# Kernel optimization log

Hardware: AMD Instinct MI355X
Metric: run time of the kernel (lower is better)

## Reference

```python
import jax, jax.numpy as jnp
import numpy as np

B, R, M, L, H = 256, 2048, 65536, 64, 4  # batch, reservoir, memory_size, key_len, read_heads


def setup_inputs() -> dict:
    key = jax.random.key(0)
    ks = jax.random.split(key, 4)
    s = 1.0 / np.sqrt(R).astype(np.float32)  # ~xavier scale for Linear weights
    return {
        "reservoir_state": jax.random.normal(ks[0], (B, R), dtype=jnp.float32),
        "memory": jax.random.normal(ks[1], (1, M, L), dtype=jnp.float32),
        "Wk": jax.random.normal(ks[2], (H * L, R), dtype=jnp.float32) * s,
        "bk": jnp.zeros((H * L,), dtype=jnp.float32),
        "Wb": jax.random.normal(ks[3], (H, R), dtype=jnp.float32) * s,
        "bb": jnp.zeros((H,), dtype=jnp.float32),
    }


def reference(reservoir_state, memory, Wk, bk, Wb, bb):
    b = reservoir_state.shape[0]
    h = Wb.shape[0]
    # key projection -> [B, H, L]
    keys = (reservoir_state @ Wk.T + bk).reshape(b, h, -1)
    # per-head key strength, relu-gated -> [B, H]
    betas = jax.nn.relu(reservoir_state @ Wb.T + bb)
    # content addressing: dot(keys, memory rows) -> [B, H, M]
    dots = jnp.einsum('bhl,ml->bhm', keys, memory[0])
    # normalize by key norm (as in original: sqrt(sum(keys^2)))
    dots = dots / jnp.sqrt(jnp.sum(keys ** 2, axis=-1, keepdims=True))
    # beta-scaled softmax over memory slots
    return jax.nn.softmax(betas[:, :, None] * dots, axis=-1)
```

## Files before the change

kernel.cpp:

```cpp
#include <hip/hip_runtime.h>
#include <hip/hip_bf16.h>

#define BB   256
#define RR   2048
#define MM   65536
#define LL   64
#define HH   4
#define NROW 1024
#define KEYS 256

typedef float f32x4 __attribute__((ext_vector_type(4)));
typedef short short8 __attribute__((ext_vector_type(8)));

#define MFMA(A,B,C) __builtin_amdgcn_mfma_f32_16x16x32_bf16((A),(B),(C),0,0,0)
#define LOG2E 1.4426950408889634f
#define EXP2F(x) __builtin_amdgcn_exp2f(x)

__device__ __forceinline__ void lds_barrier() {
    asm volatile("s_waitcnt lgkmcnt(0)" ::: "memory");
    __builtin_amdgcn_sched_barrier(0);
    __builtin_amdgcn_s_barrier();
    __builtin_amdgcn_sched_barrier(0);
}

__device__ __forceinline__ unsigned short bf16_rn(float x) {
    union { float f; unsigned int u; } v; v.f = x;
    unsigned int r = v.u + 0x7FFFu + ((v.u >> 16) & 1u);
    return (unsigned short)(r >> 16);
}
__device__ __forceinline__ float bf16_to_f(unsigned short h) {
    union { float f; unsigned int u; } v; v.u = ((unsigned int)h) << 16; return v.f;
}
__device__ __forceinline__ void split8_store(const float* x, unsigned short* hi, unsigned short* lo) {
    unsigned int ph[4], pl[4];
#pragma unroll
    for (int j = 0; j < 4; ++j) {
        unsigned short h0 = bf16_rn(x[2*j]),   l0 = bf16_rn(x[2*j]   - bf16_to_f(h0));
        unsigned short h1 = bf16_rn(x[2*j+1]), l1 = bf16_rn(x[2*j+1] - bf16_to_f(h1));
        ph[j] = (unsigned int)h0 | ((unsigned int)h1 << 16);
        pl[j] = (unsigned int)l0 | ((unsigned int)l1 << 16);
    }
    ((uint4*)hi)[0] = make_uint4(ph[0], ph[1], ph[2], ph[3]);
    ((uint4*)lo)[0] = make_uint4(pl[0], pl[1], pl[2], pl[3]);
}
__device__ __forceinline__ void split8_reg(const float* x, short8& hi, short8& lo) {
    union { unsigned int u[4]; short8 s; } H, L;
#pragma unroll
    for (int j = 0; j < 4; ++j) {
        unsigned short h0 = bf16_rn(x[2*j]),   l0 = bf16_rn(x[2*j]   - bf16_to_f(h0));
        unsigned short h1 = bf16_rn(x[2*j+1]), l1 = bf16_rn(x[2*j+1] - bf16_to_f(h1));
        H.u[j] = (unsigned int)h0 | ((unsigned int)h1 << 16);
        L.u[j] = (unsigned int)l0 | ((unsigned int)l1 << 16);
    }
    hi = H.s; lo = L.s;
}

__global__ __launch_bounds__(256) void setup_k(const float* __restrict__ mem,
                                               const float* __restrict__ Wk,
                                               const float* __restrict__ S,
                                               unsigned short* __restrict__ bhi,
                                               unsigned short* __restrict__ blo,
                                               float* __restrict__ normpart,
                                               float* __restrict__ kpart) {
    __shared__ float sh[18496];
    int bx = blockIdx.x, tid = threadIdx.x;
    if (bx < 512) {
        float* t     = sh;
        float* rowsq = sh + 128 * 68;
        int blk = bx;
        const f32x4* src = (const f32x4*)(mem + (size_t)blk * 128 * LL);
#pragma unroll
        for (int i = 0; i < 8; ++i) {
            int idx = i * 256 + tid;
            int row = idx >> 4, c4 = idx & 15;
            *(f32x4*)&t[row * 68 + c4 * 4] = src[idx];
        }
        __syncthreads();
        if (tid < 128) {
            const float* rp = t + tid * 68;
            float s = 0.f;
#pragma unroll
            for (int k = 0; k < 64; ++k) s = fmaf(rp[k], rp[k], s);
            rowsq[tid] = s;
        }
        __syncthreads();
        if (tid < 64) {
            float m = fmaxf(rowsq[tid], rowsq[tid + 64]);
#pragma unroll
            for (int off = 1; off < 64; off <<= 1) m = fmaxf(m, __shfl_xor(m, off, 64));
            if (tid == 0) normpart[blk] = m;
        }
#pragma unroll
        for (int i = 0; i < 4; ++i) {
            int slot = i * 256 + tid;
            int lane = slot & 63, frag_l = slot >> 6;
            int t_l = frag_l >> 1, c = frag_l & 1;
            int row = t_l * 16 + (lane & 15);
            int k0 = c * 32 + (lane >> 4) * 8;
            const float* p = t + row * 68 + k0;
            float x[8];
#pragma unroll
            for (int j = 0; j < 8; ++j) x[j] = p[j];
            size_t gslot = ((size_t)blk * 16 + frag_l) * 64 + lane;
            split8_store(x, bhi + gslot * 8, blo + gslot * 8);
        }
    } else {
        float* sl = sh;
        float* wk = sh + 2048;
        int bx2 = bx - 512;
        int bg = bx2 >> 3, kc = bx2 & 7;
        int b0 = bg * 8;
#pragma unroll
        for (int bi = 0; bi < 8; ++bi)
            sl[bi * 256 + tid] = S[(size_t)(b0 + bi) * RR + kc * 256 + tid];
        float acc[8] = {0,0,0,0,0,0,0,0};
        for (int sub = 0; sub < 4; ++sub) {
            const f32x4* wsrc = (const f32x4*)(Wk + (size_t)tid * RR + kc * 256 + sub * 64);
#pragma unroll
            for (int i = 0; i < 16; ++i) {
                f32x4 v = wsrc[i];
#pragma unroll
                for (int q = 0; q < 4; ++q)
                    wk[(i * 4 + q) * 257 + tid] = v[q];
            }
            __syncthreads();
#pragma unroll 4
            for (int kkl = 0; kkl < 64; ++kkl) {
                float wv = wk[kkl * 257 + tid];
                int kk = sub * 64 + kkl;
#pragma unroll
                for (int bi = 0; bi < 8; ++bi)
                    acc[bi] = fmaf(sl[bi * 256 + kk], wv, acc[bi]);
            }
            __syncthreads();
        }
        float* op = kpart + (size_t)kc * BB * KEYS + (size_t)b0 * KEYS + tid;
#pragma unroll
        for (int bi = 0; bi < 8; ++bi)
            op[bi * KEYS] = acc[bi];
    }
}

__global__ __launch_bounds__(256) void k1_finalize(const float* __restrict__ S,
                                                   const float* __restrict__ kpart,
                                                   const float* __restrict__ bk,
                                                   const float* __restrict__ Wb,
                                                   const float* __restrict__ bb,
                                                   const float* __restrict__ normpart,
                                                   float* __restrict__ q_rm,
                                                   float* __restrict__ brow) {
    int bh = blockIdx.x, b = bh >> 2, h = bh & 3;
    int tid = threadIdx.x, lane = tid & 63, w = tid >> 6;
    float p = 0.f;
#pragma unroll
    for (int i = 0; i < 8; ++i) {
        int k = i * 256 + tid;
        p += S[(size_t)b * RR + k] * Wb[(size_t)h * RR + k];
    }
    float nm = fmaxf(normpart[tid], normpart[256 + tid]);
#pragma unroll
    for (int off = 1; off < 64; off <<= 1) {
        p  += __shfl_xor(p, off, 64);
        nm  = fmaxf(nm, __shfl_xor(nm, off, 64));
    }
    __shared__ float red[4], redm[4];
    if (lane == 0) { red[w] = p; redm[w] = nm; }
    __syncthreads();
    if (tid < 64) {
        float beta = red[0] + red[1] + red[2] + red[3] + bb[h];
        beta = fmaxf(beta, 0.f);
        float maxn = sqrtf(fmaxf(fmaxf(redm[0], redm[1]), fmaxf(redm[2], redm[3])));
        float kv = bk[h * LL + lane];
#pragma unroll
        for (int c = 0; c < 8; ++c)
            kv += kpart[(size_t)c * BB * KEYS + (size_t)b * KEYS + h * LL + lane];
        float sq = kv * kv;
#pragma unroll
        for (int off = 1; off < 64; off <<= 1) sq += __shfl_xor(sq, off, 64);
        float scale = beta * LOG2E / sqrtf(sq);
        q_rm[(size_t)bh * LL + lane] = kv * scale;
        if (lane == 0) brow[bh] = beta * maxn * LOG2E;
    }
}

__device__ __forceinline__ void decode_wg(int bx, int& mblk, int& rg) {
    int wg = ((bx & 7) << 7) | (bx >> 3);
    mblk = wg >> 4; rg = wg & 15;
}

__global__ __launch_bounds__(256) void k2_mfma(const unsigned short* __restrict__ bhi,
                                               const unsigned short* __restrict__ blo,
                                               const float* __restrict__ q_rm,
                                               const float* __restrict__ brow,
                                               float* __restrict__ psum) {
    int mblk, rg; decode_wg(blockIdx.x, mblk, rg);
    int tid = threadIdx.x, w = tid >> 6, lane = tid & 63;
    int g = lane >> 4;
    short8 Ah[4][2], Al[4][2];
#pragma unroll
    for (int rt = 0; rt < 4; ++rt)
#pragma unroll
        for (int c = 0; c < 2; ++c) {
            const float* qp = q_rm + (size_t)(rg * 64 + rt * 16 + (lane & 15)) * LL
                              + c * 32 + (lane >> 4) * 8;
            f32x4 x0 = *(const f32x4*)qp, x1 = *(const f32x4*)(qp + 4);
            float x[8] = {x0[0], x0[1], x0[2], x0[3], x1[0], x1[1], x1[2], x1[3]};
            split8_reg(x, Ah[rt][c], Al[rt][c]);
        }
    float br[4][4];
#pragma unroll
    for (int rt = 0; rt < 4; ++rt)
#pragma unroll
        for (int r = 0; r < 4; ++r)
            br[rt][r] = brow[rg * 64 + rt * 16 + g * 4 + r];
    float s[4][4] = {{0.f}};
    int t0 = mblk * 64 + w * 16;
    short8 Bh0, Bh1, Bl0, Bl1;
    {
        size_t o = (size_t)t0 * 1024 + (size_t)lane * 8;
        Bh0 = *(const short8*)(bhi + o); Bh1 = *(const short8*)(bhi + o + 512);
        Bl0 = *(const short8*)(blo + o); Bl1 = *(const short8*)(blo + o + 512);
    }
#pragma unroll 4
    for (int ti = 0; ti < 16; ++ti) {
        int tn = t0 + ((ti < 15) ? ti + 1 : 15);
        size_t on = (size_t)tn * 1024 + (size_t)lane * 8;
        short8 nh0 = *(const short8*)(bhi + on);
        short8 nh1 = *(const short8*)(bhi + on + 512);
        short8 nl0 = *(const short8*)(blo + on);
        short8 nl1 = *(const short8*)(blo + on + 512);
#pragma unroll
        for (int rt = 0; rt < 4; ++rt) {
            f32x4 C = {0.f, 0.f, 0.f, 0.f};
            C = MFMA(Ah[rt][0], Bh0, C);
            C = MFMA(Ah[rt][1], Bh1, C);
            C = MFMA(Al[rt][0], Bh0, C);
            C = MFMA(Al[rt][1], Bh1, C);
            C = MFMA(Ah[rt][0], Bl0, C);
            C = MFMA(Ah[rt][1], Bl1, C);
#pragma unroll
            for (int r = 0; r < 4; ++r)
                s[rt][r] += EXP2F(C[r] - br[rt][r]);
        }
        Bh0 = nh0; Bh1 = nh1; Bl0 = nl0; Bl1 = nl1;
    }
#pragma unroll
    for (int rt = 0; rt < 4; ++rt)
#pragma unroll
        for (int r = 0; r < 4; ++r) {
            float v = s[rt][r];
            v += __shfl_xor(v, 1, 64);
            v += __shfl_xor(v, 2, 64);
            v += __shfl_xor(v, 4, 64);
            v += __shfl_xor(v, 8, 64);
            s[rt][r] = v;
        }
    if ((lane & 15) == 0) {
        int col = mblk * 4 + w;
#pragma unroll
        for (int rt = 0; rt < 4; ++rt)
#pragma unroll
            for (int r = 0; r < 4; ++r) {
                int row = rg * 64 + rt * 16 + g * 4 + r;
                psum[(size_t)row * 256 + col] = s[rt][r];
            }
    }
}

__global__ __launch_bounds__(256) void k4_mfma(const unsigned short* __restrict__ bhi,
                                               const unsigned short* __restrict__ blo,
                                               const float* __restrict__ q_rm,
                                               const float* __restrict__ brow,
                                               const float* __restrict__ psum,
                                               float* __restrict__ out) {
    __shared__ float ot[16 * 516];
    __shared__ float gsh[16];
    int bx = blockIdx.x;
    int wg = ((bx & 7) << 7) | (bx >> 3);
    int mblk = wg >> 6, rg = wg & 63;
    int tid = threadIdx.x, w = tid >> 6, lane = tid & 63;
    int g = lane >> 4;
    {
        int row16 = tid >> 4, seg = tid & 15;
        const float* pp = psum + (size_t)(rg * 16 + row16) * 256 + seg * 16;
        float part = 0.f;
#pragma unroll
        for (int j = 0; j < 16; ++j) part += pp[j];
#pragma unroll
        for (int off = 1; off < 16; off <<= 1) part += __shfl_xor(part, off, 64);
        if (seg == 0) gsh[row16] = 1.0f / part;
    }
    short8 Ah[2], Al[2];
#pragma unroll
    for (int c = 0; c < 2; ++c) {
        const float* qp = q_rm + (size_t)(rg * 16 + (lane & 15)) * LL
                          + c * 32 + (lane >> 4) * 8;
        f32x4 x0 = *(const f32x4*)qp, x1 = *(const f32x4*)(qp + 4);
        float x[8] = {x0[0], x0[1], x0[2], x0[3], x1[0], x1[1], x1[2], x1[3]};
        split8_reg(x, Ah[c], Al[c]);
    }
    __syncthreads();
    float br[4], gv[4];
#pragma unroll
    for (int r = 0; r < 4; ++r) {
        int row = rg * 16 + g * 4 + r;
        br[r] = brow[row];
        gv[r] = gsh[g * 4 + r];
    }
    int tbase = mblk * 256 + w * 8;
    short8 Bh0, Bh1, Bl0, Bl1;
    {
        size_t o = (size_t)tbase * 1024 + (size_t)lane * 8;
        Bh0 = *(const short8*)(bhi + o); Bh1 = *(const short8*)(bhi + o + 512);
        Bl0 = *(const short8*)(blo + o); Bl1 = *(const short8*)(blo + o + 512);
    }
    for (int c = 0; c < 8; ++c) {
#pragma unroll
        for (int k = 0; k < 8; ++k) {
            int j = c * 8 + k;
            int jn = (j < 63) ? j + 1 : 63;
            int tn = tbase + (jn >> 3) * 32 + (jn & 7);
            size_t on = (size_t)tn * 1024 + (size_t)lane * 8;
            short8 nh0 = *(const short8*)(bhi + on);
            short8 nh1 = *(const short8*)(bhi + on + 512);
            short8 nl0 = *(const short8*)(blo + on);
            short8 nl1 = *(const short8*)(blo + on + 512);
            f32x4 C = {0.f, 0.f, 0.f, 0.f};
            C = MFMA(Ah[0], Bh0, C);
            C = MFMA(Ah[1], Bh1, C);
            C = MFMA(Al[0], Bh0, C);
            C = MFMA(Al[1], Bh1, C);
            C = MFMA(Ah[0], Bl0, C);
            C = MFMA(Ah[1], Bl1, C);
            int cbase = w * 128 + k * 16 + (lane & 15);
#pragma unroll
            for (int r = 0; r < 4; ++r)
                ot[(g * 4 + r) * 516 + cbase] = EXP2F(C[r] - br[r]) * gv[r];
            Bh0 = nh0; Bh1 = nh1; Bl0 = nl0; Bl1 = nl1;
        }
        lds_barrier();
        size_t gbase = (size_t)mblk * 4096 + (size_t)c * 512;
#pragma unroll
        for (int i = 0; i < 8; ++i) {
            int flat = i * 256 + tid;
            int rl = flat >> 7, slot = flat & 127;
            f32x4 v = *(const f32x4*)&ot[rl * 516 + slot * 4];
            float* dst = out + (size_t)(rg * 16 + rl) * MM + gbase + (size_t)slot * 4;
            __builtin_nontemporal_store(v, (f32x4*)dst);
        }
        lds_barrier();
    }
}

extern "C" void kernel_launch(void* const* d_in, const int* in_sizes, int n_in,
                              void* d_out, int out_size, void* d_ws, size_t ws_size,
                              hipStream_t stream) {
    const float* S   = (const float*)d_in[0];
    const float* mem = (const float*)d_in[1];
    const float* Wk  = (const float*)d_in[2];
    const float* bk  = (const float*)d_in[3];
    const float* Wb  = (const float*)d_in[4];
    const float* bb  = (const float*)d_in[5];
    float* out = (float*)d_out;

    float* kpart    = (float*)d_ws;
    float* q_rm     = kpart + (size_t)8 * BB * KEYS;
    float* psum     = q_rm  + (size_t)NROW * LL;
    float* brow     = psum  + (size_t)NROW * 256;
    float* normpart = brow  + NROW;
    unsigned short* bhi = (unsigned short*)(normpart + 512);
    unsigned short* blo = bhi + (size_t)8192 * 512;

    setup_k    <<<768,  256, 0, stream>>>(mem, Wk, S, bhi, blo, normpart, kpart);
    k1_finalize<<<NROW, 256, 0, stream>>>(S, kpart, bk, Wb, bb, normpart, q_rm, brow);
    k2_mfma    <<<1024, 256, 0, stream>>>(bhi, blo, q_rm, brow, psum);
    k4_mfma    <<<1024, 256, 0, stream>>>(bhi, blo, q_rm, brow, psum, out);
}
```

Before: 359.2 us.

## Retile k4 to 64 query rows per block for memory-tile reuse

The output kernel now processes 64 query rows per workgroup instead of 16, covering half as many memory slots per block, and launches 512 blocks instead of 1024. Each loaded bf16 hi/lo memory fragment feeds four row-tiles of MFMAs, cutting repeated global reads of the memory matrix by about four times. The cost is more registers for the A fragments and the per-row constants, a larger LDS staging buffer, and fewer blocks. That may reduce occupancy on a store-bound kernel.

```diff
diff --git a/kernel.cpp b/kernel.cpp
--- a/kernel.cpp
+++ b/kernel.cpp
@@ -273,41 +273,46 @@
                                                const float* __restrict__ brow,
                                                const float* __restrict__ psum,
                                                float* __restrict__ out) {
-    __shared__ float ot[16 * 516];
-    __shared__ float gsh[16];
+    __shared__ float ot[64 * 260];
+    __shared__ float gsh[64];
     int bx = blockIdx.x;
-    int wg = ((bx & 7) << 7) | (bx >> 3);
-    int mblk = wg >> 6, rg = wg & 63;
+    int wg = ((bx & 7) << 6) | (bx >> 3);
+    int mblk = wg >> 4, rg = wg & 15;
     int tid = threadIdx.x, w = tid >> 6, lane = tid & 63;
     int g = lane >> 4;
+    int row0 = rg * 64;
     {
-        int row16 = tid >> 4, seg = tid & 15;
-        const float* pp = psum + (size_t)(rg * 16 + row16) * 256 + seg * 16;
+        int r64 = tid >> 2, seg = tid & 3;
+        const f32x4* pp = (const f32x4*)(psum + (size_t)(row0 + r64) * 256 + seg * 64);
         float part = 0.f;
 #pragma unroll
-        for (int j = 0; j < 16; ++j) part += pp[j];
-#pragma unroll
-        for (int off = 1; off < 16; off <<= 1) part += __shfl_xor(part, off, 64);
-        if (seg == 0) gsh[row16] = 1.0f / part;
-    }
-    short8 Ah[2], Al[2];
-#pragma unroll
-    for (int c = 0; c < 2; ++c) {
-        const float* qp = q_rm + (size_t)(rg * 16 + (lane & 15)) * LL
-                          + c * 32 + (lane >> 4) * 8;
-        f32x4 x0 = *(const f32x4*)qp, x1 = *(const f32x4*)(qp + 4);
-        float x[8] = {x0[0], x0[1], x0[2], x0[3], x1[0], x1[1], x1[2], x1[3]};
-        split8_reg(x, Ah[c], Al[c]);
-    }
+        for (int j = 0; j < 16; ++j) { f32x4 v = pp[j]; part += v[0] + v[1] + v[2] + v[3]; }
+        part += __shfl_xor(part, 1, 64);
+        part += __shfl_xor(part, 2, 64);
+        if (seg == 0) gsh[r64] = 1.0f / part;
+    }
+    short8 Ah[4][2], Al[4][2];
+#pragma unroll
+    for (int rt = 0; rt < 4; ++rt)
+#pragma unroll
+        for (int c = 0; c < 2; ++c) {
+            const float* qp = q_rm + (size_t)(row0 + rt * 16 + (lane & 15)) * LL
+                              + c * 32 + (lane >> 4) * 8;
+            f32x4 x0 = *(const f32x4*)qp, x1 = *(const f32x4*)(qp + 4);
+            float x[8] = {x0[0], x0[1], x0[2], x0[3], x1[0], x1[1], x1[2], x1[3]};
+            split8_reg(x, Ah[rt][c], Al[rt][c]);
+        }
     __syncthreads();
-    float br[4], gv[4];
-#pragma unroll
-    for (int r = 0; r < 4; ++r) {
-        int row = rg * 16 + g * 4 + r;
-        br[r] = brow[row];
-        gv[r] = gsh[g * 4 + r];
-    }
-    int tbase = mblk * 256 + w * 8;
+    float br[4][4], gv[4][4];
+#pragma unroll
+    for (int rt = 0; rt < 4; ++rt)
+#pragma unroll
+        for (int r = 0; r < 4; ++r) {
+            int rl = rt * 16 + g * 4 + r;
+            br[rt][r] = brow[row0 + rl];
+            gv[rt][r] = gsh[rl];
+        }
+    int tbase = mblk * 128 + w * 4;
     short8 Bh0, Bh1, Bl0, Bl1;
     {
         size_t o = (size_t)tbase * 1024 + (size_t)lane * 8;
@@ -316,36 +321,40 @@
     }
     for (int c = 0; c < 8; ++c) {
 #pragma unroll
-        for (int k = 0; k < 8; ++k) {
-            int j = c * 8 + k;
-            int jn = (j < 63) ? j + 1 : 63;
-            int tn = tbase + (jn >> 3) * 32 + (jn & 7);
+        for (int k = 0; k < 4; ++k) {
+            int j = c * 4 + k;
+            int jn = (j < 31) ? j + 1 : 31;
+            int tn = tbase + (jn >> 2) * 16 + (jn & 3);
             size_t on = (size_t)tn * 1024 + (size_t)lane * 8;
             short8 nh0 = *(const short8*)(bhi + on);
             short8 nh1 = *(const short8*)(bhi + on + 512);
             short8 nl0 = *(const short8*)(blo + on);
             short8 nl1 = *(const short8*)(blo + on + 512);
-            f32x4 C = {0.f, 0.f, 0.f, 0.f};
-            C = MFMA(Ah[0], Bh0, C);
-            C = MFMA(Ah[1], Bh1, C);
-            C = MFMA(Al[0], Bh0, C);
-            C = MFMA(Al[1], Bh1, C);
-            C = MFMA(Ah[0], Bl0, C);
-            C = MFMA(Ah[1], Bl1, C);
-            int cbase = w * 128 + k * 16 + (lane & 15);
-#pragma unroll
-            for (int r = 0; r < 4; ++r)
-                ot[(g * 4 + r) * 516 + cbase] = EXP2F(C[r] - br[r]) * gv[r];
+            int cbase = (w * 4 + k) * 16 + (lane & 15);
+#pragma unroll
+            for (int rt = 0; rt < 4; ++rt) {
+                f32x4 C = {0.f, 0.f, 0.f, 0.f};
+                C = MFMA(Ah[rt][0], Bh0, C);
+                C = MFMA(Ah[rt][1], Bh1, C);
+                C = MFMA(Al[rt][0], Bh0, C);
+                C = MFMA(Al[rt][1], Bh1, C);
+                C = MFMA(Ah[rt][0], Bl0, C);
+                C = MFMA(Ah[rt][1], Bl1, C);
+#pragma unroll
+                for (int r = 0; r < 4; ++r)
+                    ot[(rt * 16 + g * 4 + r) * 260 + cbase] =
+                        EXP2F(C[r] - br[rt][r]) * gv[rt][r];
+            }
             Bh0 = nh0; Bh1 = nh1; Bl0 = nl0; Bl1 = nl1;
         }
         lds_barrier();
-        size_t gbase = (size_t)mblk * 4096 + (size_t)c * 512;
-#pragma unroll
-        for (int i = 0; i < 8; ++i) {
+        size_t gbase = (size_t)mblk * 2048 + (size_t)c * 256;
+#pragma unroll
+        for (int i = 0; i < 16; ++i) {
             int flat = i * 256 + tid;
-            int rl = flat >> 7, slot = flat & 127;
-            f32x4 v = *(const f32x4*)&ot[rl * 516 + slot * 4];
-            float* dst = out + (size_t)(rg * 16 + rl) * MM + gbase + (size_t)slot * 4;
+            int rl = flat >> 6, slot = flat & 63;
+            f32x4 v = *(const f32x4*)&ot[rl * 260 + slot * 4];
+            float* dst = out + (size_t)(row0 + rl) * MM + gbase + (size_t)slot * 4;
             __builtin_nontemporal_store(v, (f32x4*)dst);
         }
         lds_barrier();
@@ -374,5 +383,5 @@
     setup_k    <<<768,  256, 0, stream>>>(mem, Wk, S, bhi, blo, normpart, kpart);
     k1_finalize<<<NROW, 256, 0, stream>>>(S, kpart, bk, Wb, bb, normpart, q_rm, brow);
     k2_mfma    <<<1024, 256, 0, stream>>>(bhi, blo, q_rm, brow, psum);
-    k4_mfma    <<<1024, 256, 0, stream>>>(bhi, blo, q_rm, brow, psum, out);
-}
+    k4_mfma    <<<512,  256, 0, stream>>>(bhi, blo, q_rm, brow, psum, out);
+}
```

Result: slower. 385.0 us (+7.2%).
